# Optimization experiments

Hardware: AMD Instinct MI355X
Metric: run time of the kernel (lower is better)

## Reference

```python
import jax, jax.numpy as jnp
import numpy as np

N = 100000       # num_nodes
E = 1600000      # num_edges (avg degree 16)
EL = 200000      # link-prediction edges
IN_C = 64
POS = 16
HID = 64
OUT = 32


def setup_inputs() -> dict:
    key = jax.random.key(0)
    ks = jax.random.split(key, 10)
    def glorot(k, shape):
        scale = 1.0 / np.sqrt(shape[0])
        return jax.random.uniform(k, shape, jnp.float32, -scale, scale)
    return {
        "x": jax.random.normal(ks[0], (N, IN_C), jnp.float32),
        "pos_emb": jax.random.normal(ks[1], (N, POS), jnp.float32),
        "W1": glorot(ks[2], (IN_C + POS, HID)),
        "b1": jnp.zeros((HID,), jnp.float32),
        "W2": glorot(ks[3], (HID, OUT)),
        "b2": jnp.zeros((OUT,), jnp.float32),
        "Wl": glorot(ks[4], (2 * OUT, 1)),
        "bl": jnp.zeros((1,), jnp.float32),
        "edge_index": jax.random.randint(ks[5], (2, E), 0, N, jnp.int32),
        "edge_label_index": jax.random.randint(ks[6], (2, EL), 0, N, jnp.int32),
    }


def reference(x, pos_emb, W1, b1, W2, b2, Wl, bl, edge_index, edge_label_index):
    n = x.shape[0]
    # GCNConv: add self-loops, symmetric deg^{-1/2} normalization (PyG defaults)
    loops = jnp.arange(n, dtype=edge_index.dtype)
    src = jnp.concatenate([edge_index[0], loops])  # [E+N]
    dst = jnp.concatenate([edge_index[1], loops])  # [E+N]
    deg = jax.ops.segment_sum(jnp.ones_like(dst, jnp.float32), dst, num_segments=n)
    dinv = jnp.where(deg > 0, jax.lax.rsqrt(jnp.maximum(deg, 1e-12)), 0.0)
    norm = dinv[src] * dinv[dst]  # [E+N]

    def gcn_conv(h, W, b):
        hw = h @ W                                    # [N, d_out] transform first
        msg = hw[src] * norm[:, None]                 # gather + normalize
        return jax.ops.segment_sum(msg, dst, num_segments=n) + b  # scatter-add

    h = jnp.concatenate([x, pos_emb], axis=1)         # [N, in+pos]
    h = jax.nn.relu(gcn_conv(h, W1, b1))              # dropout is eval no-op
    z = gcn_conv(h, W2, b2)                           # [N, out]

    s, d = edge_label_index[0], edge_label_index[1]
    zc = jnp.concatenate([z[s], z[d]], axis=1)        # [EL, 2*out]
    edge_pred = (zc @ Wl + bl)[:, 0]                  # [EL]
    return z, edge_pred
```

## Files before the change

### kernel.cpp

```cpp
#include <hip/hip_runtime.h>
#include <hip/hip_fp16.h>

#define NN 100000
#define NE 1600000
#define NEL 200000
#define TM 64

#define NBUCK 196
#define CAPB  10240
#define TPE   8192
#define NPART 196

typedef short s16x8 __attribute__((ext_vector_type(8)));
typedef float f32x4 __attribute__((ext_vector_type(4)));

__device__ __forceinline__ unsigned short bf16hi(float v) {
    unsigned u = __float_as_uint(v);
    return (unsigned short)((u + 0x7FFFu + ((u >> 16) & 1u)) >> 16);
}
__device__ __forceinline__ float bf16tof(unsigned short b) {
    return __uint_as_float(((unsigned)b) << 16);
}

union CsrSmem {
    struct { int hist[NBUCK], base[NBUCK], rk[NBUCK]; } p;
    struct { int cnts[256], hist[512], loff[512], ssum[256], csrbuf[CAPB]; } b;
};
__global__ __launch_bounds__(256) void k_csr(const int* __restrict__ src,
                                             const int* __restrict__ dst,
                                             int* __restrict__ gcur,
                                             int* __restrict__ bar,
                                             int* __restrict__ part,
                                             int* __restrict__ csr,
                                             int* __restrict__ off,
                                             float* __restrict__ dinv) {
    __shared__ CsrSmem sm;
    int tid = threadIdx.x;
    int b = blockIdx.x;
    for (int i = tid; i < NBUCK; i += 256) { sm.p.hist[i] = 0; sm.p.rk[i] = 0; }
    __syncthreads();
    int e0 = b * TPE;
    int e1 = min(e0 + TPE, NE);
    for (int e = e0 + tid; e < e1; e += 256)
        atomicAdd(&sm.p.hist[dst[e] >> 9], 1);
    __syncthreads();
    for (int i = tid; i < NBUCK; i += 256)
        sm.p.base[i] = i * CAPB + atomicAdd(&gcur[i], sm.p.hist[i]);
    __syncthreads();
    for (int e = e0 + tid; e < e1; e += 256) {
        int d = dst[e];
        int s = src[e];
        int bk = d >> 9;
        int r = atomicAdd(&sm.p.rk[bk], 1);
        part[sm.p.base[bk] + r] = ((d & 511) << 17) | s;
    }
    __syncthreads();
    if (tid == 0) {
        __threadfence();
        __hip_atomic_fetch_add(bar, 1, __ATOMIC_RELEASE, __HIP_MEMORY_SCOPE_AGENT);
        while (__hip_atomic_load(bar, __ATOMIC_ACQUIRE, __HIP_MEMORY_SCOPE_AGENT) < NPART)
            __builtin_amdgcn_s_sleep(16);
        __threadfence();
    }
    __syncthreads();
    sm.b.cnts[tid] = (tid < NBUCK) ? gcur[tid] : 0;
    __syncthreads();
    for (int st = 1; st < 256; st <<= 1) {
        int tmp = (tid >= st) ? sm.b.cnts[tid - st] : 0;
        __syncthreads();
        sm.b.cnts[tid] += tmp;
        __syncthreads();
    }
    int obase = (b == 0) ? 0 : sm.b.cnts[b - 1];
    int cnt = gcur[b];
    int pbase = b * CAPB;
    sm.b.hist[tid] = 0; sm.b.hist[tid + 256] = 0;
    __syncthreads();
    for (int i = tid; i < cnt; i += 256)
        atomicAdd(&sm.b.hist[part[pbase + i] >> 17], 1);
    __syncthreads();
    int a0 = sm.b.hist[2 * tid], a1 = sm.b.hist[2 * tid + 1];
    int pairs = a0 + a1;
    sm.b.ssum[tid] = pairs;
    __syncthreads();
    for (int st = 1; st < 256; st <<= 1) {
        int tmp = (tid >= st) ? sm.b.ssum[tid - st] : 0;
        __syncthreads();
        sm.b.ssum[tid] += tmp;
        __syncthreads();
    }
    int pexcl = sm.b.ssum[tid] - pairs;
    sm.b.loff[2 * tid] = pexcl;
    sm.b.loff[2 * tid + 1] = pexcl + a0;
    __syncthreads();
    for (int i = tid; i < 512; i += 256) {
        int d = b * 512 + i;
        if (d < NN) {
            int c = sm.b.hist[i];
            off[d] = obase + sm.b.loff[i] + c;
            dinv[d] = rsqrtf((float)(c + 1));
        }
    }
    sm.b.hist[tid] = 0; sm.b.hist[tid + 256] = 0;
    __syncthreads();
    for (int i = tid; i < cnt; i += 256) {
        int rec = part[pbase + i];
        int dl = rec >> 17;
        int r = atomicAdd(&sm.b.hist[dl], 1);
        sm.b.csrbuf[sm.b.loff[dl] + r] = rec & 0x1FFFF;
    }
    __syncthreads();
    for (int i = tid; i < cnt; i += 256)
        csr[obase + i] = sm.b.csrbuf[i];
}

#define HW1_K 104
__global__ __launch_bounds__(256) void k_hw1(const float* __restrict__ x,
                                             const float* __restrict__ pos,
                                             const float* __restrict__ W1,
                                             const float* __restrict__ dinv,
                                             __half* __restrict__ hw1) {
    __shared__ unsigned short ahi[64 * HW1_K];
    __shared__ unsigned short alo[64 * HW1_K];
    __shared__ unsigned short bhi[64 * HW1_K];
    __shared__ unsigned short blo[64 * HW1_K];
    __shared__ float sdin[64];
    int tid = threadIdx.x;
    int nb = blockIdx.x * 64;
    for (int i = tid; i < 64 * 24; i += 256) {
        int r = i / 24, c = i - r * 24;
        ahi[r * HW1_K + 80 + c] = 0; alo[r * HW1_K + 80 + c] = 0;
        bhi[r * HW1_K + 80 + c] = 0; blo[r * HW1_K + 80 + c] = 0;
    }
    for (int i = tid; i < 64 * 64; i += 256) {
        int r = i >> 6, c = i & 63;
        int g = nb + r;
        float v = (g < NN) ? x[g * 64 + c] : 0.0f;
        unsigned short h = bf16hi(v);
        ahi[r * HW1_K + c] = h;
        alo[r * HW1_K + c] = bf16hi(v - bf16tof(h));
    }
    for (int i = tid; i < 64 * 16; i += 256) {
        int r = i >> 4, c = i & 15;
        int g = nb + r;
        float v = (g < NN) ? pos[g * 16 + c] : 0.0f;
        unsigned short h = bf16hi(v);
        ahi[r * HW1_K + 64 + c] = h;
        alo[r * HW1_K + 64 + c] = bf16hi(v - bf16tof(h));
    }
    for (int i = tid; i < 80 * 64; i += 256) {
        int k = i >> 6, c = i & 63;
        float v = W1[i];
        unsigned short h = bf16hi(v);
        bhi[c * HW1_K + k] = h;
        blo[c * HW1_K + k] = bf16hi(v - bf16tof(h));
    }
    for (int i = tid; i < 64; i += 256) {
        int g = nb + i;
        sdin[i] = (g < NN) ? dinv[g] : 0.0f;
    }
    __syncthreads();
    int wave = tid >> 6, lane = tid & 63;
    int frow = lane & 15, fq = lane >> 4;
    int r0 = wave * 16;
    int aoff = (r0 + frow) * HW1_K + fq * 8;
    s16x8 ah0 = *(s16x8*)&ahi[aoff];
    s16x8 ah1 = *(s16x8*)&ahi[aoff + 32];
    s16x8 ah2 = *(s16x8*)&ahi[aoff + 64];
    s16x8 al0 = *(s16x8*)&alo[aoff];
    s16x8 al1 = *(s16x8*)&alo[aoff + 32];
    s16x8 al2 = *(s16x8*)&alo[aoff + 64];
    f32x4 acc[4];
#pragma unroll
    for (int ct = 0; ct < 4; ++ct) {
        acc[ct] = (f32x4)(0.0f);
        int boff = (ct * 16 + frow) * HW1_K + fq * 8;
        s16x8 bh0 = *(s16x8*)&bhi[boff];
        s16x8 bh1 = *(s16x8*)&bhi[boff + 32];
        s16x8 bh2 = *(s16x8*)&bhi[boff + 64];
        s16x8 bl0 = *(s16x8*)&blo[boff];
        s16x8 bl1 = *(s16x8*)&blo[boff + 32];
        s16x8 bl2 = *(s16x8*)&blo[boff + 64];
        acc[ct] = __builtin_amdgcn_mfma_f32_16x16x32_bf16(ah0, bh0, acc[ct], 0, 0, 0);
        acc[ct] = __builtin_amdgcn_mfma_f32_16x16x32_bf16(ah1, bh1, acc[ct], 0, 0, 0);
        acc[ct] = __builtin_amdgcn_mfma_f32_16x16x32_bf16(ah2, bh2, acc[ct], 0, 0, 0);
        acc[ct] = __builtin_amdgcn_mfma_f32_16x16x32_bf16(ah0, bl0, acc[ct], 0, 0, 0);
        acc[ct] = __builtin_amdgcn_mfma_f32_16x16x32_bf16(ah1, bl1, acc[ct], 0, 0, 0);
        acc[ct] = __builtin_amdgcn_mfma_f32_16x16x32_bf16(ah2, bl2, acc[ct], 0, 0, 0);
        acc[ct] = __builtin_amdgcn_mfma_f32_16x16x32_bf16(al0, bh0, acc[ct], 0, 0, 0);
        acc[ct] = __builtin_amdgcn_mfma_f32_16x16x32_bf16(al1, bh1, acc[ct], 0, 0, 0);
        acc[ct] = __builtin_amdgcn_mfma_f32_16x16x32_bf16(al2, bh2, acc[ct], 0, 0, 0);
    }
#pragma unroll
    for (int ct = 0; ct < 4; ++ct) {
        int col = ct * 16 + frow;
#pragma unroll
        for (int i = 0; i < 4; ++i) {
            int r = r0 + fq * 4 + i;
            int g = nb + r;
            if (g < NN)
                hw1[g * 64 + col] = __float2half_rn(acc[ct][i] * sdin[r]);
        }
    }
}

__global__ __launch_bounds__(256) void k_gather1(const int* __restrict__ off,
                                                 const int* __restrict__ csr,
                                                 const float* __restrict__ dinv,
                                                 const __half* __restrict__ hw,
                                                 const float* __restrict__ b1,
                                                 const float* __restrict__ W2,
                                                 __half* __restrict__ hw2out) {
    __shared__ float h2row[4][64];
    int tid = threadIdx.x;
    int lane = tid & 63;
    int wave = tid >> 6;
    int d = blockIdx.x * 4 + wave;
    int start = (d == 0) ? 0 : off[d - 1];
    int end = off[d];
    start = __builtin_amdgcn_readfirstlane(start);
    end   = __builtin_amdgcn_readfirstlane(end);
    float dd = dinv[d];
    float hself = __half2float(hw[d * 64 + lane]);
    float acc0 = 0.0f, acc1 = 0.0f, acc2 = 0.0f, acc3 = 0.0f;
    for (int e = start; e < end; e += 16) {
        int rem = end - e;
        int s0 = csr[e];
        int s1  = (rem > 1)  ? csr[e + 1]  : s0;
        int s2  = (rem > 2)  ? csr[e + 2]  : s0;
        int s3  = (rem > 3)  ? csr[e + 3]  : s0;
        int s4  = (rem > 4)  ? csr[e + 4]  : s0;
        int s5  = (rem > 5)  ? csr[e + 5]  : s0;
        int s6  = (rem > 6)  ? csr[e + 6]  : s0;
        int s7  = (rem > 7)  ? csr[e + 7]  : s0;
        int s8  = (rem > 8)  ? csr[e + 8]  : s0;
        int s9  = (rem > 9)  ? csr[e + 9]  : s0;
        int s10 = (rem > 10) ? csr[e + 10] : s0;
        int s11 = (rem > 11) ? csr[e + 11] : s0;
        int s12 = (rem > 12) ? csr[e + 12] : s0;
        int s13 = (rem > 13) ? csr[e + 13] : s0;
        int s14 = (rem > 14) ? csr[e + 14] : s0;
        int s15 = (rem > 15) ? csr[e + 15] : s0;
        float g0  = __half2float(hw[s0  * 64 + lane]);
        float g1  = __half2float(hw[s1  * 64 + lane]);
        float g2  = __half2float(hw[s2  * 64 + lane]);
        float g3  = __half2float(hw[s3  * 64 + lane]);
        float g4  = __half2float(hw[s4  * 64 + lane]);
        float g5  = __half2float(hw[s5  * 64 + lane]);
        float g6  = __half2float(hw[s6  * 64 + lane]);
        float g7  = __half2float(hw[s7  * 64 + lane]);
        float g8  = __half2float(hw[s8  * 64 + lane]);
        float g9  = __half2float(hw[s9  * 64 + lane]);
        float g10 = __half2float(hw[s10 * 64 + lane]);
        float g11 = __half2float(hw[s11 * 64 + lane]);
        float g12 = __half2float(hw[s12 * 64 + lane]);
        float g13 = __half2float(hw[s13 * 64 + lane]);
        float g14 = __half2float(hw[s14 * 64 + lane]);
        float g15 = __half2float(hw[s15 * 64 + lane]);
        int inv = 16 - rem;
        if (inv < 0) inv = 0;
        acc0 += g0;  acc1 += g1;  acc2 += g2;  acc3 += g3;
        acc0 += g4;  acc1 += g5;  acc2 += g6;  acc3 += g7;
        acc0 += g8;  acc1 += g9;  acc2 += g10; acc3 += g11;
        acc0 += g12; acc1 += g13; acc2 += g14; acc3 += g15;
        acc3 = fmaf(-(float)inv, g0, acc3);
    }
    float v = fmaxf(b1[lane] + dd * (((acc0 + acc1) + (acc2 + acc3)) + hself), 0.0f);
    h2row[wave][lane] = v;
    int j = lane & 31;
    int half = lane >> 5;
    float sum = 0.0f;
#pragma unroll
    for (int k = 0; k < 32; ++k) {
        int kk = half * 32 + k;
        sum += h2row[wave][kk] * W2[kk * 32 + j];
    }
    sum += __shfl_xor(sum, 32, 64);
    if (half == 0)
        hw2out[d * 32 + j] = __float2half_rn(sum * dd);
}

__global__ __launch_bounds__(256) void k_gather2(const int* __restrict__ off,
                                                 const int* __restrict__ csr,
                                                 const float* __restrict__ dinv,
                                                 const __half* __restrict__ hw,
                                                 const float* __restrict__ b2,
                                                 const float* __restrict__ Wl,
                                                 float* __restrict__ outz,
                                                 float* __restrict__ uu,
                                                 float* __restrict__ vv) {
    int lane = threadIdx.x & 63;
    int half = lane >> 5;
    int j = lane & 31;
    int wave = threadIdx.x >> 6;
    int d = blockIdx.x * 4 + wave;
    int start = (d == 0) ? 0 : off[d - 1];
    int end = off[d];
    start = __builtin_amdgcn_readfirstlane(start);
    end   = __builtin_amdgcn_readfirstlane(end);
    float dd = dinv[d];
    float hself = __half2float(hw[d * 32 + j]);
    float accA = 0.0f, accB = 0.0f, accC = 0.0f, accD = 0.0f;
    for (int e = start; e < end; e += 16) {
        int rem = end - e;
        int s0 = csr[e];
        int i1 = e + half;
        int sA = (half      < rem) ? csr[i1]      : s0;
        int sB = (half + 2  < rem) ? csr[i1 + 2]  : s0;
        int sC = (half + 4  < rem) ? csr[i1 + 4]  : s0;
        int sD = (half + 6  < rem) ? csr[i1 + 6]  : s0;
        int sE = (half + 8  < rem) ? csr[i1 + 8]  : s0;
        int sF = (half + 10 < rem) ? csr[i1 + 10] : s0;
        int sG = (half + 12 < rem) ? csr[i1 + 12] : s0;
        int sH = (half + 14 < rem) ? csr[i1 + 14] : s0;
        float gA = __half2float(hw[sA * 32 + j]);
        float gB = __half2float(hw[sB * 32 + j]);
        float gC = __half2float(hw[sC * 32 + j]);
        float gD = __half2float(hw[sD * 32 + j]);
        float gE = __half2float(hw[sE * 32 + j]);
        float gF = __half2float(hw[sF * 32 + j]);
        float gG = __half2float(hw[sG * 32 + j]);
        float gH = __half2float(hw[sH * 32 + j]);
        int nv = (rem - half + 1) >> 1;
        if (nv > 8) nv = 8;
        int inv = 8 - nv;
        accA += gA; accB += gB; accC += gC; accD += gD;
        accA += gE; accB += gF; accC += gG; accD += gH;
        accD = fmaf(-(float)inv, gH, accD);
    }
    float acc = (accA + accB) + (accC + accD);
    acc += __shfl(acc, lane ^ 32, 64);
    float z = b2[j] + dd * (acc + hself);
    if (half == 0)
        outz[d * 32 + j] = z;
    float p0 = z * Wl[j];
    float p1 = z * Wl[32 + j];
    p0 += __shfl_xor(p0, 1, 64);  p1 += __shfl_xor(p1, 1, 64);
    p0 += __shfl_xor(p0, 2, 64);  p1 += __shfl_xor(p1, 2, 64);
    p0 += __shfl_xor(p0, 4, 64);  p1 += __shfl_xor(p1, 4, 64);
    p0 += __shfl_xor(p0, 8, 64);  p1 += __shfl_xor(p1, 8, 64);
    p0 += __shfl_xor(p0, 16, 64); p1 += __shfl_xor(p1, 16, 64);
    if (lane == 0) { uu[d] = p0; vv[d] = p1; }
}

__global__ __launch_bounds__(256) void k_linkpred(const int* __restrict__ sidx,
                                                  const int* __restrict__ didx,
                                                  const float* __restrict__ uu,
                                                  const float* __restrict__ vv,
                                                  const float* __restrict__ bl,
                                                  float* __restrict__ pred) {
    int e = blockIdx.x * 256 + threadIdx.x;
    if (e < NEL)
        pred[e] = uu[sidx[e]] + vv[didx[e]] + bl[0];
}

extern "C" void kernel_launch(void* const* d_in, const int* in_sizes, int n_in,
                              void* d_out, int out_size, void* d_ws, size_t ws_size,
                              hipStream_t stream) {
    const float* x    = (const float*)d_in[0];
    const float* pos  = (const float*)d_in[1];
    const float* W1   = (const float*)d_in[2];
    const float* b1   = (const float*)d_in[3];
    const float* W2   = (const float*)d_in[4];
    const float* b2   = (const float*)d_in[5];
    const float* Wl   = (const float*)d_in[6];
    const float* bl   = (const float*)d_in[7];
    const int*   ei   = (const int*)d_in[8];
    const int*   eli  = (const int*)d_in[9];
    const int* src  = ei;
    const int* dst  = ei + NE;
    const int* lsrc = eli;
    const int* ldst = eli + NEL;

    float* out_z    = (float*)d_out;
    float* out_pred = (float*)d_out + NN * 32;

    float*  dinv  = (float*)d_ws;
    int*    off   = (int*)(dinv + NN);
    int*    gcur  = off + NN;
    int*    bar   = gcur + NBUCK;
    int*    csr   = bar + 1;
    __half* hw1   = (__half*)(csr + NE);
    int*    part  = (int*)hw1;
    __half* hw2   = hw1 + NN * 64;
    float*  uu    = (float*)(hw2 + NN * 32);
    float*  vv    = uu + NN;

    hipMemsetAsync(gcur, 0, (NBUCK + 1) * sizeof(int), stream);

    k_csr<<<NPART, 256, 0, stream>>>(src, dst, gcur, bar, part, csr, off, dinv);

    k_hw1<<<(NN + TM - 1) / TM, 256, 0, stream>>>(x, pos, W1, dinv, hw1);

    k_gather1<<<NN / 4, 256, 0, stream>>>(off, csr, dinv, hw1, b1, W2, hw2);

    k_gather2<<<NN / 4, 256, 0, stream>>>(off, csr, dinv, hw2, b2, Wl,
                                          out_z, uu, vv);

    k_linkpred<<<(NEL + 255) / 256, 256, 0, stream>>>(lsrc, ldst, uu, vv, bl,
                                                      out_pred);
}
```

Baseline: 299.7 us.

## Replace bucketed CSR build with atomic degree count and atomic scatter

Replaces the single-kernel two-pass bucket sort, which relied on a grid-wide spin barrier, with three steps: a global-atomic degree histogram, a per-block row-offset allocation folded into the hw1 GEMM kernel, and an atomic-cursor scatter of source ids. Row offsets are allocated per 64-node block through an atomic on a running total, so CSR rows are not in node order and neighbor order within a row is nondeterministic. The gather kernels now read rowstart and degree and compute dinv inline. This trades the barrier and the shared-memory sort for many contended global atomics and random writes to csr.

```diff
diff --git a/kernel.cpp b/kernel.cpp
--- a/kernel.cpp
+++ b/kernel.cpp
@@ -6,11 +6,6 @@
 #define NEL 200000
 #define TM 64
 
-#define NBUCK 196
-#define CAPB  10240
-#define TPE   8192
-#define NPART 196
-
 typedef short s16x8 __attribute__((ext_vector_type(8)));
 typedef float f32x4 __attribute__((ext_vector_type(4)));
 
@@ -22,103 +17,41 @@
     return __uint_as_float(((unsigned)b) << 16);
 }
 
-union CsrSmem {
-    struct { int hist[NBUCK], base[NBUCK], rk[NBUCK]; } p;
-    struct { int cnts[256], hist[512], loff[512], ssum[256], csrbuf[CAPB]; } b;
-};
-__global__ __launch_bounds__(256) void k_csr(const int* __restrict__ src,
-                                             const int* __restrict__ dst,
-                                             int* __restrict__ gcur,
-                                             int* __restrict__ bar,
-                                             int* __restrict__ part,
-                                             int* __restrict__ csr,
-                                             int* __restrict__ off,
-                                             float* __restrict__ dinv) {
-    __shared__ CsrSmem sm;
-    int tid = threadIdx.x;
-    int b = blockIdx.x;
-    for (int i = tid; i < NBUCK; i += 256) { sm.p.hist[i] = 0; sm.p.rk[i] = 0; }
-    __syncthreads();
-    int e0 = b * TPE;
-    int e1 = min(e0 + TPE, NE);
-    for (int e = e0 + tid; e < e1; e += 256)
-        atomicAdd(&sm.p.hist[dst[e] >> 9], 1);
-    __syncthreads();
-    for (int i = tid; i < NBUCK; i += 256)
-        sm.p.base[i] = i * CAPB + atomicAdd(&gcur[i], sm.p.hist[i]);
-    __syncthreads();
-    for (int e = e0 + tid; e < e1; e += 256) {
-        int d = dst[e];
-        int s = src[e];
-        int bk = d >> 9;
-        int r = atomicAdd(&sm.p.rk[bk], 1);
-        part[sm.p.base[bk] + r] = ((d & 511) << 17) | s;
-    }
-    __syncthreads();
-    if (tid == 0) {
-        __threadfence();
-        __hip_atomic_fetch_add(bar, 1, __ATOMIC_RELEASE, __HIP_MEMORY_SCOPE_AGENT);
-        while (__hip_atomic_load(bar, __ATOMIC_ACQUIRE, __HIP_MEMORY_SCOPE_AGENT) < NPART)
-            __builtin_amdgcn_s_sleep(16);
-        __threadfence();
-    }
-    __syncthreads();
-    sm.b.cnts[tid] = (tid < NBUCK) ? gcur[tid] : 0;
-    __syncthreads();
-    for (int st = 1; st < 256; st <<= 1) {
-        int tmp = (tid >= st) ? sm.b.cnts[tid - st] : 0;
-        __syncthreads();
-        sm.b.cnts[tid] += tmp;
-        __syncthreads();
-    }
-    int obase = (b == 0) ? 0 : sm.b.cnts[b - 1];
-    int cnt = gcur[b];
-    int pbase = b * CAPB;
-    sm.b.hist[tid] = 0; sm.b.hist[tid + 256] = 0;
-    __syncthreads();
-    for (int i = tid; i < cnt; i += 256)
-        atomicAdd(&sm.b.hist[part[pbase + i] >> 17], 1);
-    __syncthreads();
-    int a0 = sm.b.hist[2 * tid], a1 = sm.b.hist[2 * tid + 1];
-    int pairs = a0 + a1;
-    sm.b.ssum[tid] = pairs;
-    __syncthreads();
-    for (int st = 1; st < 256; st <<= 1) {
-        int tmp = (tid >= st) ? sm.b.ssum[tid - st] : 0;
-        __syncthreads();
-        sm.b.ssum[tid] += tmp;
-        __syncthreads();
-    }
-    int pexcl = sm.b.ssum[tid] - pairs;
-    sm.b.loff[2 * tid] = pexcl;
-    sm.b.loff[2 * tid + 1] = pexcl + a0;
-    __syncthreads();
-    for (int i = tid; i < 512; i += 256) {
-        int d = b * 512 + i;
-        if (d < NN) {
-            int c = sm.b.hist[i];
-            off[d] = obase + sm.b.loff[i] + c;
-            dinv[d] = rsqrtf((float)(c + 1));
-        }
-    }
-    sm.b.hist[tid] = 0; sm.b.hist[tid + 256] = 0;
-    __syncthreads();
-    for (int i = tid; i < cnt; i += 256) {
-        int rec = part[pbase + i];
-        int dl = rec >> 17;
-        int r = atomicAdd(&sm.b.hist[dl], 1);
-        sm.b.csrbuf[sm.b.loff[dl] + r] = rec & 0x1FFFF;
-    }
-    __syncthreads();
-    for (int i = tid; i < cnt; i += 256)
-        csr[obase + i] = sm.b.csrbuf[i];
+__global__ __launch_bounds__(256) void k_deg(const int* __restrict__ dst,
+                                             int* __restrict__ deg) {
+    int e4 = (blockIdx.x * 256 + threadIdx.x) * 4;
+    if (e4 < NE) {
+        int4 d = *(const int4*)&dst[e4];
+        atomicAdd(&deg[d.x], 1);
+        atomicAdd(&deg[d.y], 1);
+        atomicAdd(&deg[d.z], 1);
+        atomicAdd(&deg[d.w], 1);
+    }
+}
+
+__global__ __launch_bounds__(256) void k_scatter(const int* __restrict__ src,
+                                                 const int* __restrict__ dst,
+                                                 int* __restrict__ cur,
+                                                 int* __restrict__ csr) {
+    int e4 = (blockIdx.x * 256 + threadIdx.x) * 4;
+    if (e4 < NE) {
+        int4 d = *(const int4*)&dst[e4];
+        int4 s = *(const int4*)&src[e4];
+        csr[atomicAdd(&cur[d.x], 1)] = s.x;
+        csr[atomicAdd(&cur[d.y], 1)] = s.y;
+        csr[atomicAdd(&cur[d.z], 1)] = s.z;
+        csr[atomicAdd(&cur[d.w], 1)] = s.w;
+    }
 }
 
 #define HW1_K 104
 __global__ __launch_bounds__(256) void k_hw1(const float* __restrict__ x,
                                              const float* __restrict__ pos,
                                              const float* __restrict__ W1,
-                                             const float* __restrict__ dinv,
+                                             const int* __restrict__ deg,
+                                             int* __restrict__ total,
+                                             int* __restrict__ rowstart,
+                                             int* __restrict__ cur,
                                              __half* __restrict__ hw1) {
     __shared__ unsigned short ahi[64 * HW1_K];
     __shared__ unsigned short alo[64 * HW1_K];
@@ -127,6 +60,26 @@
     __shared__ float sdin[64];
     int tid = threadIdx.x;
     int nb = blockIdx.x * 64;
+    if (tid < 64) {
+        int g = nb + tid;
+        int di = (g < NN) ? deg[g] : 0;
+        int incl = di;
+#pragma unroll
+        for (int o = 1; o < 64; o <<= 1) {
+            int t = __shfl_up(incl, o, 64);
+            if (tid >= o) incl += t;
+        }
+        int excl = incl - di;
+        int bsum = __shfl(incl, 63, 64);
+        int base = 0;
+        if (tid == 0) base = atomicAdd(total, bsum);
+        base = __shfl(base, 0, 64);
+        if (g < NN) {
+            rowstart[g] = base + excl;
+            cur[g] = base + excl;
+            sdin[tid] = rsqrtf((float)(di + 1));
+        }
+    }
     for (int i = tid; i < 64 * 24; i += 256) {
         int r = i / 24, c = i - r * 24;
         ahi[r * HW1_K + 80 + c] = 0; alo[r * HW1_K + 80 + c] = 0;
@@ -154,10 +107,6 @@
         unsigned short h = bf16hi(v);
         bhi[c * HW1_K + k] = h;
         blo[c * HW1_K + k] = bf16hi(v - bf16tof(h));
-    }
-    for (int i = tid; i < 64; i += 256) {
-        int g = nb + i;
-        sdin[i] = (g < NN) ? dinv[g] : 0.0f;
     }
     __syncthreads();
     int wave = tid >> 6, lane = tid & 63;
@@ -204,9 +153,9 @@
     }
 }
 
-__global__ __launch_bounds__(256) void k_gather1(const int* __restrict__ off,
+__global__ __launch_bounds__(256) void k_gather1(const int* __restrict__ rowstart,
+                                                 const int* __restrict__ deg,
                                                  const int* __restrict__ csr,
-                                                 const float* __restrict__ dinv,
                                                  const __half* __restrict__ hw,
                                                  const float* __restrict__ b1,
                                                  const float* __restrict__ W2,
@@ -216,11 +165,11 @@
     int lane = tid & 63;
     int wave = tid >> 6;
     int d = blockIdx.x * 4 + wave;
-    int start = (d == 0) ? 0 : off[d - 1];
-    int end = off[d];
+    int start = rowstart[d];
+    int dg = deg[d];
     start = __builtin_amdgcn_readfirstlane(start);
-    end   = __builtin_amdgcn_readfirstlane(end);
-    float dd = dinv[d];
+    int end = start + __builtin_amdgcn_readfirstlane(dg);
+    float dd = rsqrtf((float)(dg + 1));
     float hself = __half2float(hw[d * 64 + lane]);
     float acc0 = 0.0f, acc1 = 0.0f, acc2 = 0.0f, acc3 = 0.0f;
     for (int e = start; e < end; e += 16) {
@@ -280,9 +229,9 @@
         hw2out[d * 32 + j] = __float2half_rn(sum * dd);
 }
 
-__global__ __launch_bounds__(256) void k_gather2(const int* __restrict__ off,
+__global__ __launch_bounds__(256) void k_gather2(const int* __restrict__ rowstart,
+                                                 const int* __restrict__ deg,
                                                  const int* __restrict__ csr,
-                                                 const float* __restrict__ dinv,
                                                  const __half* __restrict__ hw,
                                                  const float* __restrict__ b2,
                                                  const float* __restrict__ Wl,
@@ -294,11 +243,11 @@
     int j = lane & 31;
     int wave = threadIdx.x >> 6;
     int d = blockIdx.x * 4 + wave;
-    int start = (d == 0) ? 0 : off[d - 1];
-    int end = off[d];
+    int start = rowstart[d];
+    int dg = deg[d];
     start = __builtin_amdgcn_readfirstlane(start);
-    end   = __builtin_amdgcn_readfirstlane(end);
-    float dd = dinv[d];
+    int end = start + __builtin_amdgcn_readfirstlane(dg);
+    float dd = rsqrtf((float)(dg + 1));
     float hself = __half2float(hw[d * 32 + j]);
     float accA = 0.0f, accB = 0.0f, accC = 0.0f, accD = 0.0f;
     for (int e = start; e < end; e += 16) {
@@ -375,26 +324,28 @@
     float* out_z    = (float*)d_out;
     float* out_pred = (float*)d_out + NN * 32;
 
-    float*  dinv  = (float*)d_ws;
-    int*    off   = (int*)(dinv + NN);
-    int*    gcur  = off + NN;
-    int*    bar   = gcur + NBUCK;
-    int*    csr   = bar + 1;
-    __half* hw1   = (__half*)(csr + NE);
-    int*    part  = (int*)hw1;
+    int*    deg   = (int*)d_ws;
+    int*    total = deg + NN;
+    int*    rowstart = total + 1;
+    int*    cur   = rowstart + NN;
+    int*    csr   = cur + NN;
+    __half* hw1   = (__half*)(csr + NE + 16);
     __half* hw2   = hw1 + NN * 64;
     float*  uu    = (float*)(hw2 + NN * 32);
     float*  vv    = uu + NN;
 
-    hipMemsetAsync(gcur, 0, (NBUCK + 1) * sizeof(int), stream);
-
-    k_csr<<<NPART, 256, 0, stream>>>(src, dst, gcur, bar, part, csr, off, dinv);
-
-    k_hw1<<<(NN + TM - 1) / TM, 256, 0, stream>>>(x, pos, W1, dinv, hw1);
-
-    k_gather1<<<NN / 4, 256, 0, stream>>>(off, csr, dinv, hw1, b1, W2, hw2);
-
-    k_gather2<<<NN / 4, 256, 0, stream>>>(off, csr, dinv, hw2, b2, Wl,
+    hipMemsetAsync(deg, 0, (NN + 1) * sizeof(int), stream);
+
+    k_deg<<<(NE / 4 + 255) / 256, 256, 0, stream>>>(dst, deg);
+
+    k_hw1<<<(NN + TM - 1) / TM, 256, 0, stream>>>(x, pos, W1, deg, total,
+                                                  rowstart, cur, hw1);
+
+    k_scatter<<<(NE / 4 + 255) / 256, 256, 0, stream>>>(src, dst, cur, csr);
+
+    k_gather1<<<NN / 4, 256, 0, stream>>>(rowstart, deg, csr, hw1, b1, W2, hw2);
+
+    k_gather2<<<NN / 4, 256, 0, stream>>>(rowstart, deg, csr, hw2, b2, Wl,
                                           out_z, uu, vv);
 
     k_linkpred<<<(NEL + 255) / 256, 256, 0, stream>>>(lsrc, ldst, uu, vv, bl,
```

Result: slower. 431.3 us (+43.9%).
